# Performance work log

Measured on AMD Instinct MI355X. Metric: run time of the kernel, lower is better.

The kernel has to match this reference:

```python
import jax, jax.numpy as jnp
import numpy as np

B, C, L = 32, 64, 4096
HIDDEN = 64
SR = 50.0
KS = (7, 15, 31, 63)
PHYS = 12
EPS_BN = 1e-5
EPS_GN = 1e-5


def _dwconv(x, w):
    # x: (B,C,L), w: (C,1,k) depthwise kernel, SAME padding for odd k
    k = w.shape[-1]
    p = (k - 1) // 2
    return jax.lax.conv_general_dilated(
        x, w, window_strides=(1,), padding=[(p, p)],
        dimension_numbers=('NCH', 'OIH', 'NCH'),
        feature_group_count=x.shape[1])


def _physics(x):
    b, c, l = x.shape
    svm = jnp.sqrt((x * x).sum(axis=1))                      # (B,L) channel norm
    svm_max = svm.max(axis=-1)
    svm_mean = svm.mean(axis=-1)
    svm_std = jnp.std(svm, axis=-1, ddof=1) + 1e-6           # torch.std is unbiased
    jerk = jnp.diff(x, axis=-1) * SR                         # (B,C,L-1)
    jerk_max = jnp.abs(jerk).max(axis=-1).mean(axis=-1)      # (B,)
    jerk_rate = jnp.diff(jerk, axis=-1) * SR
    jerk_rate_max = jnp.abs(jerk_rate).max(axis=-1).mean(axis=-1)
    sign_changes = (x[:, :, :-1] * x[:, :, 1:] < 0).astype(x.dtype)
    zcr = sign_changes.sum(axis=-1).mean(axis=-1) / l
    thr = (svm_mean + 2.0 * svm_std)[:, None]
    impact_duration = (svm > thr).astype(x.dtype).sum(axis=-1) / l
    hthr = (svm_mean + 3.0 * svm_std)[:, None]
    impact_ratio = (svm > hthr).astype(x.dtype).sum(axis=-1) / l
    free_fall = (svm < (svm_mean - svm_std)[:, None]).astype(x.dtype).sum(axis=-1) / l
    second_half = svm[:, l // 2:]
    post_stillness = jnp.tanh(1.0 / (jnp.std(second_half, axis=-1, ddof=1) + 1e-6))
    third = max(1, l // 3)
    pre_mean = svm[:, :third].mean(axis=-1)
    impact_peak = svm[:, third:2 * third].max(axis=-1)
    post_mean = svm[:, 2 * third:].mean(axis=-1)
    fall_phase = jax.nn.relu(impact_peak - pre_mean) + jax.nn.relu(impact_peak - post_mean)
    fall_phase = fall_phase / (jnp.abs(impact_peak) + 1e-6)
    spectrum = jnp.fft.rfft(x.astype(jnp.float32), axis=-1, norm='ortho')
    power = (jnp.abs(spectrum) ** 2).sum(axis=1)             # (B, L//2+1)
    freqs = jnp.linspace(0.0, 1.0, power.shape[-1], dtype=power.dtype)
    total_power = power.sum(axis=-1) + 1e-6
    spectral_centroid = (power * freqs).sum(axis=-1) / total_power
    high_freq_ratio = jnp.where(freqs > 0.4, power, 0.0).sum(axis=-1) / total_power
    feats = jnp.stack([svm_max, svm_mean, jerk_max, jerk_rate_max, zcr,
                       impact_duration, impact_ratio, post_stillness, free_fall,
                       spectral_centroid, high_freq_ratio, fall_phase], axis=-1)
    return jnp.nan_to_num(feats, nan=0.0, posinf=0.0, neginf=0.0).astype(x.dtype)


def _forward(x, dw_w7, dw_w15, dw_w31, dw_w63, bn_g, bn_b, bn_m, bn_v,
             comp_w1, comp_b1, comp_w2, comp_b2,
             pn_g, pn_b, pn_m, pn_v,
             pe_w1, pe_b1, pe_w2, pe_b2, pg_w, pg_b,
             temperature, gn_g, gn_b, proj_w, proj_b, res_scale):
    # 4 depthwise conv + BN(eval) branches
    branches = []
    for i, w in enumerate((dw_w7, dw_w15, dw_w31, dw_w63)):
        y = _dwconv(x, w)
        y = (y - bn_m[i][None, :, None]) / jnp.sqrt(bn_v[i][None, :, None] + EPS_BN) \
            * bn_g[i][None, :, None] + bn_b[i][None, :, None]
        branches.append(y)
    stacked = jnp.stack(branches, axis=1)                    # (B,4,C,L)
    # complexity net: global avg pool -> MLP
    xm = x.mean(axis=-1)                                     # (B,C)
    h = jax.nn.relu(xm @ comp_w1 + comp_b1)
    complexity_logits = h @ comp_w2 + comp_b2                # (B,4)
    # physics gate
    pf = _physics(x)                                         # (B,12)
    pf = (pf - pn_m) / jnp.sqrt(pn_v + EPS_BN) * pn_g + pn_b
    pe = jax.nn.relu(jax.nn.relu(pf @ pe_w1 + pe_b1) @ pe_w2 + pe_b2)
    physics_weights = jax.nn.sigmoid(pe @ pg_w + pg_b)       # (B,4)
    temp = jnp.maximum(temperature, 0.1)
    weights = jax.nn.softmax(complexity_logits * physics_weights / temp, axis=-1)
    mixed = jnp.einsum('bkcl,bk->bcl', stacked, weights)
    # proj: GroupNorm(1,C) -> GELU(exact) -> 1x1 conv
    mu = mixed.mean(axis=(1, 2), keepdims=True)
    var = mixed.var(axis=(1, 2), keepdims=True)
    gn = (mixed - mu) / jnp.sqrt(var + EPS_GN) * gn_g[None, :, None] + gn_b[None, :, None]
    act = jax.nn.gelu(gn, approximate=False)
    out = jnp.einsum('oc,bcl->bol', proj_w, act) + proj_b[None, :, None]
    return x + res_scale * out


def setup_inputs() -> dict:
    ks = jax.random.split(jax.random.key(0), 16)
    f32 = jnp.float32
    inp = {}
    inp['x'] = jax.random.normal(ks[0], (B, C, L), dtype=f32)
    for i, k in enumerate(KS):
        inp[f'dw_w{k}'] = jax.random.normal(ks[1 + i], (C, 1, k), dtype=f32) / np.sqrt(k)
    inp['bn_g'] = jnp.ones((4, C), f32)
    inp['bn_b'] = jnp.zeros((4, C), f32)
    inp['bn_m'] = 0.1 * jax.random.normal(ks[5], (4, C), dtype=f32)
    inp['bn_v'] = jax.random.uniform(ks[6], (4, C), dtype=f32, minval=0.5, maxval=1.5)
    inp['comp_w1'] = jax.random.normal(ks[7], (C, HIDDEN), dtype=f32) / np.sqrt(C)
    inp['comp_b1'] = jnp.zeros((HIDDEN,), f32)
    inp['comp_w2'] = jax.random.normal(ks[8], (HIDDEN, 4), dtype=f32) / np.sqrt(HIDDEN)
    inp['comp_b2'] = jnp.zeros((4,), f32)
    inp['pn_g'] = jnp.ones((PHYS,), f32)
    inp['pn_b'] = jnp.zeros((PHYS,), f32)
    inp['pn_m'] = 0.1 * jax.random.normal(ks[9], (PHYS,), dtype=f32)
    inp['pn_v'] = jax.random.uniform(ks[10], (PHYS,), dtype=f32, minval=0.5, maxval=1.5)
    inp['pe_w1'] = jax.random.normal(ks[11], (PHYS, 32), dtype=f32) / np.sqrt(PHYS)
    inp['pe_b1'] = jnp.zeros((32,), f32)
    inp['pe_w2'] = jax.random.normal(ks[12], (32, 32), dtype=f32) / np.sqrt(32)
    inp['pe_b2'] = jnp.zeros((32,), f32)
    inp['pg_w'] = jax.random.normal(ks[13], (32, 4), dtype=f32) / np.sqrt(32)
    inp['pg_b'] = jnp.zeros((4,), f32)
    inp['temperature'] = jnp.asarray(1.0, f32)
    inp['gn_g'] = jnp.ones((C,), f32)
    inp['gn_b'] = jnp.zeros((C,), f32)
    inp['proj_w'] = jax.random.normal(ks[14], (C, C), dtype=f32) / np.sqrt(C)
    inp['proj_b'] = jnp.zeros((C,), f32)
    inp['res_scale'] = jnp.asarray(0.5, f32)  # init is 0.0; 0.5 gives a non-trivial output
    return inp


def reference(x, dw_w7, dw_w15, dw_w31, dw_w63, bn_g, bn_b, bn_m, bn_v,
              comp_w1, comp_b1, comp_w2, comp_b2,
              pn_g, pn_b, pn_m, pn_v,
              pe_w1, pe_b1, pe_w2, pe_b2, pg_w, pg_b,
              temperature, gn_g, gn_b, proj_w, proj_b, res_scale):
    return _forward(x, dw_w7, dw_w15, dw_w31, dw_w63, bn_g, bn_b, bn_m, bn_v,
                    comp_w1, comp_b1, comp_w2, comp_b2, pn_g, pn_b, pn_m, pn_v,
                    pe_w1, pe_b1, pe_w2, pe_b2, pg_w, pg_b,
                    temperature, gn_g, gn_b, proj_w, proj_b, res_scale)
```

## Files before the change

### kernel.cpp

```cpp
#include <hip/hip_runtime.h>
#include <math.h>

#define LN 4096
#define CN 64
#define BQ 32
#define NTH 256

#define OFF_CHAN_SUM    0
#define OFF_CHAN_JERK   2048
#define OFF_CHAN_JRATE  4096
#define OFF_CHAN_ZCR    6144
#define OFF_SVMST_PART  8192
#define OFF_SPEC_PART   12288
#define OFF_EFF_B       15360
#define OFF_GNP         17408
#define OFF_EFF_W       21504
#define OFF_SVMBUF      152576

#define FP(i) ((i) + ((i) >> 4))

__device__ __forceinline__ void bfly4(float2& a, float2& b, float2& c, float2& d,
                                      float w1r, float w1i, float w2r, float w2i,
                                      float w3r, float w3i) {
  float t1r = b.x*w1r - b.y*w1i, t1i = b.x*w1i + b.y*w1r;
  float t2r = c.x*w2r - c.y*w2i, t2i = c.x*w2i + c.y*w2r;
  float t3r = d.x*w3r - d.y*w3i, t3i = d.x*w3i + d.y*w3r;
  float ar = a.x + t2r, ai = a.y + t2i;
  float br = a.x - t2r, bi = a.y - t2i;
  float cr = t1r + t3r, ci = t1i + t3i;
  float dr = t1r - t3r, di = t1i - t3i;
  a = make_float2(ar + cr, ai + ci);
  b = make_float2(br + di, bi - dr);
  c = make_float2(ar - cr, ai - ci);
  d = make_float2(br - di, bi + dr);
}

__global__ __launch_bounds__(NTH) void kS(const float* __restrict__ x, float* __restrict__ ws) {
  __shared__ __align__(16) char smraw[34880];
  int role = blockIdx.x;
  int t = threadIdx.x;

  if (role < 2048) {
    int bc = role;
    const float* row = x + (size_t)bc * LN;
    int l0 = t * 16;
    float rd[18];
    const float4* r4 = (const float4*)(row + l0);
#pragma unroll
    for (int q = 0; q < 4; q++) {
      float4 v = r4[q];
      rd[4*q] = v.x; rd[4*q+1] = v.y; rd[4*q+2] = v.z; rd[4*q+3] = v.w;
    }
    if (t < 255) { rd[16] = row[l0 + 16]; rd[17] = row[l0 + 17]; }
    else { rd[16] = 0.f; rd[17] = 0.f; }
    float lsum = 0.f, jm = 0.f, jrm = 0.f; int zc = 0;
#pragma unroll
    for (int i = 0; i < 16; i++) {
      float a = rd[i], b2 = rd[i+1];
      lsum += a;
      int l = l0 + i;
      if (l < LN - 1) {
        jm = fmaxf(jm, fabsf(b2 - a));
        zc += (a * b2 < 0.f);
        if (l < LN - 2) jrm = fmaxf(jrm, fabsf(rd[i+2] - 2.f*b2 + a));
      }
    }
    for (int off = 32; off > 0; off >>= 1) {
      lsum += __shfl_down(lsum, off);
      jm = fmaxf(jm, __shfl_down(jm, off));
      jrm = fmaxf(jrm, __shfl_down(jrm, off));
      zc += __shfl_down(zc, off);
    }
    float* s1 = (float*)smraw; float* s2_ = s1 + 4; float* s3 = s1 + 8; int* s4 = (int*)(s1 + 12);
    int w = t >> 6;
    if ((t & 63) == 0) { s1[w] = lsum; s2_[w] = jm; s3[w] = jrm; s4[w] = zc; }
    __syncthreads();
    if (t == 0) {
      float S = 0, J = 0, JR = 0; int Z = 0;
      for (int i = 0; i < 4; i++) { S += s1[i]; J = fmaxf(J, s2_[i]); JR = fmaxf(JR, s3[i]); Z += s4[i]; }
      ws[OFF_CHAN_SUM + bc]   = S;
      ws[OFF_CHAN_JERK + bc]  = J * 50.f;
      ws[OFF_CHAN_JRATE + bc] = JR * 2500.f;
      ws[OFF_CHAN_ZCR + bc]   = (float)Z;
    }
  } else if (role < 2560) {
    int blk = role - 2048;
    int b = blk >> 4, lt = blk & 15;
    int l = lt * 256 + t;
    const float* xb = x + (size_t)b * CN * LN + l;
    float acc = 0.f;
#pragma unroll
    for (int c = 0; c < CN; c++) { float v = xb[(size_t)c * LN]; acc = fmaf(v, v, acc); }
    float svm = sqrtf(acc);
    ws[OFF_SVMBUF + (size_t)b * LN + l] = svm;
    const int third = LN / 3;
    float vS = svm, vS2 = svm * svm;
    float vS2H  = (l >= LN/2) ? svm : 0.f;
    float vS2H2 = (l >= LN/2) ? svm * svm : 0.f;
    float vPRE  = (l < third) ? svm : 0.f;
    float vPOST = (l >= 2*third) ? svm : 0.f;
    float vMX = svm;
    float vMID = (l >= third && l < 2*third) ? svm : 0.f;
    for (int off = 32; off > 0; off >>= 1) {
      vS += __shfl_down(vS, off); vS2 += __shfl_down(vS2, off);
      vS2H += __shfl_down(vS2H, off); vS2H2 += __shfl_down(vS2H2, off);
      vPRE += __shfl_down(vPRE, off); vPOST += __shfl_down(vPOST, off);
      vMX = fmaxf(vMX, __shfl_down(vMX, off));
      vMID = fmaxf(vMID, __shfl_down(vMID, off));
    }
    float (*red)[4] = (float(*)[4])smraw;
    int w = t >> 6;
    if ((t & 63) == 0) {
      red[0][w] = vS; red[1][w] = vS2; red[2][w] = vMX; red[3][w] = vS2H;
      red[4][w] = vS2H2; red[5][w] = vPRE; red[6][w] = vMID; red[7][w] = vPOST;
    }
    __syncthreads();
    if (t == 0) {
      float* sp = ws + OFF_SVMST_PART + (size_t)blk * 8;
      sp[0] = red[0][0]+red[0][1]+red[0][2]+red[0][3];
      sp[1] = red[1][0]+red[1][1]+red[1][2]+red[1][3];
      sp[2] = fmaxf(fmaxf(red[2][0],red[2][1]),fmaxf(red[2][2],red[2][3]));
      sp[3] = red[3][0]+red[3][1]+red[3][2]+red[3][3];
      sp[4] = red[4][0]+red[4][1]+red[4][2]+red[4][3];
      sp[5] = red[5][0]+red[5][1]+red[5][2]+red[5][3];
      sp[6] = fmaxf(fmaxf(red[6][0],red[6][1]),fmaxf(red[6][2],red[6][3]));
      sp[7] = red[7][0]+red[7][1]+red[7][2]+red[7][3];
    }
  } else {
    int blk = role - 2560;
    int b = blk >> 5, cp = blk & 31;
    const float* r0 = x + ((size_t)b * CN + 2 * cp) * LN;
    const float* r1 = r0 + LN;
    float2* z = (float2*)smraw;
    float (*red)[4] = (float(*)[4])(smraw + 34816);
#pragma unroll
    for (int k = 0; k < 4; k++) {
      int n4 = (k * 256 + t) * 4;
      float4 a = *(const float4*)(r0 + n4);
      float4 c = *(const float4*)(r1 + n4);
      float ar[4] = {a.x, a.y, a.z, a.w}, cr[4] = {c.x, c.y, c.z, c.w};
#pragma unroll
      for (int q = 0; q < 4; q++) {
        unsigned n = (unsigned)(n4 + q);
        unsigned br = __brev(n) >> 20;
        unsigned dr = ((br & 0x555u) << 1) | ((br & 0xAAAu) >> 1);
        z[FP(dr)] = make_float2(ar[q], cr[q]);
      }
    }
    __syncthreads();
    const float c8r[4] = { 1.f, 0.92387953251f, 0.70710678119f, 0.38268343236f };
    const float c8i[4] = { 0.f, -0.38268343236f, -0.70710678119f, -0.92387953251f };
#pragma unroll
    for (int p = 0; p < 3; p++) {
      const int H = (p == 0) ? 1 : (p == 1) ? 16 : 256;
      int r = t & (H - 1);
      int B = ((t / H) * 16 * H) + r;
      float2 E[16];
#pragma unroll
      for (int q = 0; q < 16; q++) E[q] = z[FP(B + q * H)];
      float su, cu;
      sincospif((float)r / (8.0f * (float)H), &su, &cu);
      float ur = cu, ui = -su;
      float u2r = ur*ur - ui*ui, u2i = 2.f*ur*ui;
      float w1r = u2r*u2r - u2i*u2i, w1i = 2.f*u2r*u2i;
      float w2r = w1r*w1r - w1i*w1i, w2i = 2.f*w1r*w1i;
      float w3r = w2r*w1r - w2i*w1i, w3i = w2r*w1i + w2i*w1r;
#pragma unroll
      for (int m = 0; m < 4; m++)
        bfly4(E[4*m], E[4*m+1], E[4*m+2], E[4*m+3], w1r, w1i, w2r, w2i, w3r, w3i);
#pragma unroll
      for (int m = 0; m < 4; m++) {
        float W1r = ur*c8r[m] - ui*c8i[m];
        float W1i = ur*c8i[m] + ui*c8r[m];
        float W2r = W1r*W1r - W1i*W1i, W2i = 2.f*W1r*W1i;
        float W3r = W2r*W1r - W2i*W1i, W3i = W2r*W1i + W2i*W1r;
        bfly4(E[m], E[m+4], E[m+8], E[m+12], W1r, W1i, W2r, W2i, W3r, W3i);
      }
#pragma unroll
      for (int q = 0; q < 16; q++) z[FP(B + q * H)] = E[q];
      __syncthreads();
    }
    float tot = 0.f, cen = 0.f, hi = 0.f;
    for (int k = t; k <= LN / 2; k += NTH) {
      float p;
      if (k == 0 || k == LN / 2) {
        float2 v = z[FP(k)];
        p = v.x * v.x + v.y * v.y;
      } else {
        float2 zk = z[FP(k)], zn = z[FP(LN - k)];
        float a1 = zk.x + zn.x, a2 = zk.y - zn.y, a3 = zk.y + zn.y, a4 = zk.x - zn.x;
        p = 0.25f * (a1*a1 + a2*a2 + a3*a3 + a4*a4);
      }
      p *= (1.0f / LN);
      tot += p;
      cen += p * ((float)k * (1.0f / (LN / 2)));
      if (k >= 820) hi += p;
    }
    for (int off = 32; off > 0; off >>= 1) {
      tot += __shfl_down(tot, off);
      cen += __shfl_down(cen, off);
      hi  += __shfl_down(hi, off);
    }
    int w = t >> 6;
    if ((t & 63) == 0) { red[0][w] = tot; red[1][w] = cen; red[2][w] = hi; }
    __syncthreads();
    if (t == 0) {
      float* sp = ws + OFF_SPEC_PART + (size_t)blk * 3;
      sp[0] = red[0][0]+red[0][1]+red[0][2]+red[0][3];
      sp[1] = red[1][0]+red[1][1]+red[1][2]+red[1][3];
      sp[2] = red[2][0]+red[2][1]+red[2][2]+red[2][3];
    }
  }
}

__global__ __launch_bounds__(NTH) void k4_gate(
    const float* __restrict__ dw7, const float* __restrict__ dw15,
    const float* __restrict__ dw31, const float* __restrict__ dw63,
    const float* __restrict__ bn_g, const float* __restrict__ bn_b,
    const float* __restrict__ bn_m, const float* __restrict__ bn_v,
    const float* __restrict__ comp_w1, const float* __restrict__ comp_b1,
    const float* __restrict__ comp_w2, const float* __restrict__ comp_b2,
    const float* __restrict__ pn_g, const float* __restrict__ pn_b,
    const float* __restrict__ pn_m, const float* __restrict__ pn_v,
    const float* __restrict__ pe_w1, const float* __restrict__ pe_b1,
    const float* __restrict__ pe_w2, const float* __restrict__ pe_b2,
    const float* __restrict__ pg_w, const float* __restrict__ pg_b,
    const float* __restrict__ temperature,
    float* __restrict__ ws)
{
  int b = blockIdx.x, t = threadIdx.x;
  __shared__ float sp8[16][8];
  __shared__ float sp3[32][3];
  __shared__ float stv[10];
  __shared__ float bc2[2];
  __shared__ float xm[64], h[64], pf[12], pe1v[32], pe2v[32], lgts[4], wts[4];
  __shared__ int ri[3][4], cnts[3];
  if (t < 16) {
    const float* p = ws + OFF_SVMST_PART + (size_t)(b * 16 + t) * 8;
#pragma unroll
    for (int i = 0; i < 8; i++) sp8[t][i] = p[i];
  }
  if (t >= 32 && t < 64) {
    int i = t - 32;
    const float* p = ws + OFF_SPEC_PART + (size_t)(b * 32 + i) * 3;
    sp3[i][0] = p[0]; sp3[i][1] = p[1]; sp3[i][2] = p[2];
  }
  __syncthreads();
  if (t == 0) {
    float S=0,S2=0,MX=-1e30f,S2H=0,S2H2=0,PRE=0,MID=-1e30f,POST=0;
    for (int i = 0; i < 16; i++) {
      S += sp8[i][0]; S2 += sp8[i][1]; MX = fmaxf(MX, sp8[i][2]);
      S2H += sp8[i][3]; S2H2 += sp8[i][4]; PRE += sp8[i][5];
      MID = fmaxf(MID, sp8[i][6]); POST += sp8[i][7];
    }
    float tot=0,cen=0,hi=0;
    for (int i = 0; i < 32; i++) { tot += sp3[i][0]; cen += sp3[i][1]; hi += sp3[i][2]; }
    stv[0]=S; stv[1]=S2; stv[2]=MX; stv[3]=S2H; stv[4]=S2H2;
    stv[5]=PRE; stv[6]=MID; stv[7]=POST; stv[8]=cen/(tot+1e-6f); stv[9]=hi/(tot+1e-6f);
    float mean = S * (1.f / LN);
    float var = (S2 - S * S * (1.f / LN)) * (1.f / (LN - 1));
    var = fmaxf(var, 0.f);
    bc2[0] = mean;
    bc2[1] = sqrtf(var) + 1e-6f;
  }
  __syncthreads();
  float mean = bc2[0], stde = bc2[1];
  float thr2 = mean + 2.f * stde, thr3 = mean + 3.f * stde, thrf = mean - stde;
  const float* svm = ws + OFF_SVMBUF + (size_t)b * LN;
  int c2 = 0, c3 = 0, cf = 0;
  for (int l = t; l < LN; l += NTH) {
    float v = svm[l];
    c2 += (v > thr2); c3 += (v > thr3); cf += (v < thrf);
  }
  for (int off = 32; off > 0; off >>= 1) {
    c2 += __shfl_down(c2, off); c3 += __shfl_down(c3, off); cf += __shfl_down(cf, off);
  }
  int w = t >> 6;
  if ((t & 63) == 0) { ri[0][w] = c2; ri[1][w] = c3; ri[2][w] = cf; }
  float j = 0.f, jr = 0.f, zz = 0.f;
  if (t < 64) {
    xm[t] = ws[OFF_CHAN_SUM + b * 64 + t] * (1.0f / LN);
    j  = ws[OFF_CHAN_JERK + b * 64 + t];
    jr = ws[OFF_CHAN_JRATE + b * 64 + t];
    zz = ws[OFF_CHAN_ZCR + b * 64 + t];
    for (int off = 32; off > 0; off >>= 1) {
      j += __shfl_down(j, off); jr += __shfl_down(jr, off); zz += __shfl_down(zz, off);
    }
  }
  __syncthreads();
  if (t == 0) {
    cnts[0] = ri[0][0]+ri[0][1]+ri[0][2]+ri[0][3];
    cnts[1] = ri[1][0]+ri[1][1]+ri[1][2]+ri[1][3];
    cnts[2] = ri[2][0]+ri[2][1]+ri[2][2]+ri[2][3];
    const int third = LN / 3;
    float S2H = stv[3], S2H2 = stv[4];
    float n2 = (float)(LN / 2);
    float var2 = (S2H2 - S2H * S2H / n2) / (n2 - 1.f);
    var2 = fmaxf(var2, 0.f);
    float post_still = tanhf(1.f / (sqrtf(var2) + 1e-6f));
    float pre_mean = stv[5] / (float)third;
    float post_mean = stv[7] / (float)(LN - 2 * third);
    float pk = stv[6];
    float fp = fmaxf(pk - pre_mean, 0.f) + fmaxf(pk - post_mean, 0.f);
    fp = fp / (fabsf(pk) + 1e-6f);
    pf[0] = stv[2];
    pf[1] = mean;
    pf[2] = j * (1.f / 64);
    pf[3] = jr * (1.f / 64);
    pf[4] = (zz * (1.f / 64)) * (1.f / LN);
    pf[5] = (float)cnts[0] / LN;
    pf[6] = (float)cnts[1] / LN;
    pf[7] = post_still;
    pf[8] = (float)cnts[2] / LN;
    pf[9] = stv[8];
    pf[10] = stv[9];
    pf[11] = fp;
  }
  __syncthreads();
  if (t < 12) pf[t] = (pf[t] - pn_m[t]) * rsqrtf(pn_v[t] + 1e-5f) * pn_g[t] + pn_b[t];
  __syncthreads();
  if (t < 64) {
    float hv = comp_b1[t];
    for (int i = 0; i < 64; i++) hv = fmaf(xm[i], comp_w1[i * 64 + t], hv);
    h[t] = fmaxf(hv, 0.f);
  }
  if (t < 32) {
    float v = pe_b1[t];
    for (int i = 0; i < 12; i++) v = fmaf(pf[i], pe_w1[i * 32 + t], v);
    pe1v[t] = fmaxf(v, 0.f);
  }
  __syncthreads();
  if (t < 32) {
    float v = pe_b2[t];
    for (int i = 0; i < 32; i++) v = fmaf(pe1v[i], pe_w2[i * 32 + t], v);
    pe2v[t] = fmaxf(v, 0.f);
  }
  __syncthreads();
  if (t < 4) {
    float v = comp_b2[t];
    for (int i = 0; i < 64; i++) v = fmaf(h[i], comp_w2[i * 4 + t], v);
    float g = pg_b[t];
    for (int i = 0; i < 32; i++) g = fmaf(pe2v[i], pg_w[i * 4 + t], g);
    g = 1.f / (1.f + expf(-g));
    float temp = fmaxf(temperature[0], 0.1f);
    lgts[t] = v * g / temp;
  }
  __syncthreads();
  if (t < 4) {
    float m = fmaxf(fmaxf(lgts[0], lgts[1]), fmaxf(lgts[2], lgts[3]));
    float den = expf(lgts[0]-m) + expf(lgts[1]-m) + expf(lgts[2]-m) + expf(lgts[3]-m);
    wts[t] = expf(lgts[t] - m) / den;
  }
  __syncthreads();
  if (t < 64) {
    int c = t;
    float w0 = wts[0], w1 = wts[1], w2 = wts[2], w3 = wts[3];
    float sc0 = bn_g[0*64+c] * rsqrtf(bn_v[0*64+c] + 1e-5f);
    float sc1 = bn_g[1*64+c] * rsqrtf(bn_v[1*64+c] + 1e-5f);
    float sc2 = bn_g[2*64+c] * rsqrtf(bn_v[2*64+c] + 1e-5f);
    float sc3 = bn_g[3*64+c] * rsqrtf(bn_v[3*64+c] + 1e-5f);
    float o0 = bn_b[0*64+c] - bn_m[0*64+c] * sc0;
    float o1 = bn_b[1*64+c] - bn_m[1*64+c] * sc1;
    float o2 = bn_b[2*64+c] - bn_m[2*64+c] * sc2;
    float o3 = bn_b[3*64+c] - bn_m[3*64+c] * sc3;
    ws[OFF_EFF_B + b * 64 + c] = w0*o0 + w1*o1 + w2*o2 + w3*o3;
    float a0 = w0*sc0, a1 = w1*sc1, a2 = w2*sc2, a3 = w3*sc3;
    float* eff = ws + OFF_EFF_W + (size_t)(b * 64 + c) * 64;
    for (int tau = 0; tau < 64; tau++) {
      float v = 0.f;
      if (tau < 63) {
        v = a3 * dw63[c * 63 + tau];
        int i7 = tau - 28;  if (i7 >= 0 && i7 < 7)   v = fmaf(a0, dw7[c * 7 + i7], v);
        int i15 = tau - 24; if (i15 >= 0 && i15 < 15) v = fmaf(a1, dw15[c * 15 + i15], v);
        int i31 = tau - 16; if (i31 >= 0 && i31 < 31) v = fmaf(a2, dw31[c * 31 + i31], v);
      }
      eff[tau] = v;
    }
  }
}

__device__ __forceinline__ float4 ldmask(const float* __restrict__ row, int idx) {
  int idxc = idx < 0 ? 0 : (idx > LN - 4 ? LN - 4 : idx);
  float4 v = *(const float4*)(row + idxc);
  float m = (idx == idxc) ? 1.f : 0.f;
  v.x *= m; v.y *= m; v.z *= m; v.w *= m;
  return v;
}

#define F16(wv,a0,a1,a2,a3,a4,a5,a6,a7,a8,a9,aA,aB,aC,aD,aE,aF) \
  acc[0]=fmaf(wv,a0,acc[0]);  acc[1]=fmaf(wv,a1,acc[1]);  acc[2]=fmaf(wv,a2,acc[2]);  acc[3]=fmaf(wv,a3,acc[3]);  \
  acc[4]=fmaf(wv,a4,acc[4]);  acc[5]=fmaf(wv,a5,acc[5]);  acc[6]=fmaf(wv,a6,acc[6]);  acc[7]=fmaf(wv,a7,acc[7]);  \
  acc[8]=fmaf(wv,a8,acc[8]);  acc[9]=fmaf(wv,a9,acc[9]);  acc[10]=fmaf(wv,aA,acc[10]); acc[11]=fmaf(wv,aB,acc[11]); \
  acc[12]=fmaf(wv,aC,acc[12]); acc[13]=fmaf(wv,aD,acc[13]); acc[14]=fmaf(wv,aE,acc[14]); acc[15]=fmaf(wv,aF,acc[15]);

__global__ __launch_bounds__(NTH) void k5_conv(const float* __restrict__ x,
                                               float* __restrict__ ws,
                                               float* __restrict__ mixed_out) {
  int bc = blockIdx.x;
  int t = threadIdx.x;
  __shared__ float wt[64];
  __shared__ float biasS;
  __shared__ double rda[2][4];
  if (t < 64) wt[t] = ws[OFF_EFF_W + (size_t)bc * 64 + t];
  if (t == 0) biasS = ws[OFF_EFF_B + bc];
  const float* row = x + (size_t)bc * LN;
  int l0 = t * 16;
  int g0 = l0 - 32;
  float4 R0 = ldmask(row, g0);
  float4 R1 = ldmask(row, g0 + 4);
  float4 R2 = ldmask(row, g0 + 8);
  float4 R3 = ldmask(row, g0 + 12);
  float4 R4 = ldmask(row, g0 + 16);
  __syncthreads();
  float bias = biasS;
  float acc[16];
#pragma unroll
  for (int jj = 0; jj < 16; jj++) acc[jj] = bias;
#pragma unroll
  for (int g = 0; g < 16; g++) {
    float w0 = wt[4*g], w1 = wt[4*g+1], w2 = wt[4*g+2], w3 = wt[4*g+3];
    F16(w0, R0.y,R0.z,R0.w,R1.x,R1.y,R1.z,R1.w,R2.x,R2.y,R2.z,R2.w,R3.x,R3.y,R3.z,R3.w,R4.x)
    F16(w1, R0.z,R0.w,R1.x,R1.y,R1.z,R1.w,R2.x,R2.y,R2.z,R2.w,R3.x,R3.y,R3.z,R3.w,R4.x,R4.y)
    F16(w2, R0.w,R1.x,R1.y,R1.z,R1.w,R2.x,R2.y,R2.z,R2.w,R3.x,R3.y,R3.z,R3.w,R4.x,R4.y,R4.z)
    F16(w3, R1.x,R1.y,R1.z,R1.w,R2.x,R2.y,R2.z,R2.w,R3.x,R3.y,R3.z,R3.w,R4.x,R4.y,R4.z,R4.w)
    if (g < 15) {
      R0 = R1; R1 = R2; R2 = R3; R3 = R4;
      R4 = ldmask(row, g0 + 4 * (g + 5));
    }
  }
  double ls = 0, ls2 = 0;
#pragma unroll
  for (int jj = 0; jj < 16; jj++) { float v = acc[jj]; ls += v; ls2 += (double)v * (double)v; }
  for (int off = 32; off > 0; off >>= 1) {
    ls += __shfl_down(ls, off);
    ls2 += __shfl_down(ls2, off);
  }
  int w = t >> 6;
  if ((t & 63) == 0) { rda[0][w] = ls; rda[1][w] = ls2; }
  __syncthreads();
  if (t == 0) {
    double* gp = (double*)(ws + OFF_GNP);
    gp[2 * bc + 0] = rda[0][0]+rda[0][1]+rda[0][2]+rda[0][3];
    gp[2 * bc + 1] = rda[1][0]+rda[1][1]+rda[1][2]+rda[1][3];
  }
  float* dst = mixed_out + (size_t)bc * LN + l0;
#pragma unroll
  for (int q = 0; q < 4; q++) {
    float4 v; v.x = acc[4*q]; v.y = acc[4*q+1]; v.z = acc[4*q+2]; v.w = acc[4*q+3];
    *(float4*)(dst + 4 * q) = v;
  }
}

__global__ __launch_bounds__(NTH) void k6_final(const float* __restrict__ x,
    const float* __restrict__ proj_w, const float* __restrict__ proj_b,
    const float* __restrict__ gn_g, const float* __restrict__ gn_b,
    const float* __restrict__ res_scale,
    const float* __restrict__ ws, float* out) {
  int blk = blockIdx.x;
  int b = blk >> 5;
  int l0 = (blk & 31) * 128;
  __shared__ float actS[64 * 128];
  __shared__ float Wt[64 * 64];
  __shared__ double rg[2][4];
  __shared__ float bcst[2];
  int t = threadIdx.x;
  {
    const double* gp = (const double*)(ws + OFF_GNP) + (size_t)b * CN * 2;
    double s1 = 0, s2 = 0;
    for (int i = t; i < CN; i += NTH) { s1 += gp[2*i]; s2 += gp[2*i+1]; }
    for (int off = 32; off > 0; off >>= 1) { s1 += __shfl_down(s1, off); s2 += __shfl_down(s2, off); }
    int w = t >> 6;
    if ((t & 63) == 0) { rg[0][w] = s1; rg[1][w] = s2; }
    __syncthreads();
    if (t == 0) {
      double S1 = rg[0][0]+rg[0][1]+rg[0][2]+rg[0][3];
      double S2 = rg[1][0]+rg[1][1]+rg[1][2]+rg[1][3];
      const double NN = 64.0 * 4096.0;
      double mud = S1 / NN;
      bcst[0] = (float)mud;
      bcst[1] = rsqrtf((float)(S2 / NN - mud * mud) + 1e-5f);
    }
  }
  for (int i = t; i < 4096; i += NTH) {
    int o = i & 63, c = i >> 6;
    Wt[c * 64 + o] = proj_w[o * 64 + c];
  }
  __syncthreads();
  float mu = bcst[0], rstd = bcst[1];
  const float* mx = out + (size_t)b * CN * LN;
  for (int i = t; i < 8192; i += NTH) {
    int c = i >> 7, l = i & 127;
    float v = mx[(size_t)c * LN + l0 + l];
    float g = (v - mu) * rstd * gn_g[c] + gn_b[c];
    float a = 0.5f * g * (1.f + erff(g * 0.70710678118654752f));
    actS[c * 128 + l] = a;
  }
  __syncthreads();
  int lg = t & 31;
  int og = (t >> 5) * 8;
  float4 acc4[8];
#pragma unroll
  for (int q = 0; q < 8; q++) { acc4[q].x = 0.f; acc4[q].y = 0.f; acc4[q].z = 0.f; acc4[q].w = 0.f; }
  for (int c = 0; c < 64; c++) {
    float4 a = *(const float4*)&actS[c * 128 + lg * 4];
    float4 wlo = *(const float4*)&Wt[c * 64 + og];
    float4 whi = *(const float4*)&Wt[c * 64 + og + 4];
    float wv[8] = { wlo.x, wlo.y, wlo.z, wlo.w, whi.x, whi.y, whi.z, whi.w };
#pragma unroll
    for (int q = 0; q < 8; q++) {
      acc4[q].x = fmaf(wv[q], a.x, acc4[q].x);
      acc4[q].y = fmaf(wv[q], a.y, acc4[q].y);
      acc4[q].z = fmaf(wv[q], a.z, acc4[q].z);
      acc4[q].w = fmaf(wv[q], a.w, acc4[q].w);
    }
  }
  float rsv = res_scale[0];
  const float* xb = x + (size_t)b * CN * LN;
  float* ob = out + (size_t)b * CN * LN;
#pragma unroll
  for (int q = 0; q < 8; q++) {
    int o = og + q;
    float pb = proj_b[o];
    size_t base = (size_t)o * LN + l0 + lg * 4;
    float4 xv = *(const float4*)&xb[base];
    float4 r;
    r.x = xv.x + rsv * (acc4[q].x + pb);
    r.y = xv.y + rsv * (acc4[q].y + pb);
    r.z = xv.z + rsv * (acc4[q].z + pb);
    r.w = xv.w + rsv * (acc4[q].w + pb);
    *(float4*)&ob[base] = r;
  }
}

extern "C" void kernel_launch(void* const* d_in, const int* in_sizes, int n_in,
                              void* d_out, int out_size, void* d_ws, size_t ws_size,
                              hipStream_t stream) {
  const float* x        = (const float*)d_in[0];
  const float* dw7      = (const float*)d_in[1];
  const float* dw15     = (const float*)d_in[2];
  const float* dw31     = (const float*)d_in[3];
  const float* dw63     = (const float*)d_in[4];
  const float* bn_g     = (const float*)d_in[5];
  const float* bn_b     = (const float*)d_in[6];
  const float* bn_m     = (const float*)d_in[7];
  const float* bn_v     = (const float*)d_in[8];
  const float* comp_w1  = (const float*)d_in[9];
  const float* comp_b1  = (const float*)d_in[10];
  const float* comp_w2  = (const float*)d_in[11];
  const float* comp_b2  = (const float*)d_in[12];
  const float* pn_g     = (const float*)d_in[13];
  const float* pn_b     = (const float*)d_in[14];
  const float* pn_m     = (const float*)d_in[15];
  const float* pn_v     = (const float*)d_in[16];
  const float* pe_w1    = (const float*)d_in[17];
  const float* pe_b1    = (const float*)d_in[18];
  const float* pe_w2    = (const float*)d_in[19];
  const float* pe_b2    = (const float*)d_in[20];
  const float* pg_w     = (const float*)d_in[21];
  const float* pg_b     = (const float*)d_in[22];
  const float* temperature = (const float*)d_in[23];
  const float* gn_g     = (const float*)d_in[24];
  const float* gn_b     = (const float*)d_in[25];
  const float* proj_w   = (const float*)d_in[26];
  const float* proj_b   = (const float*)d_in[27];
  const float* res_scale= (const float*)d_in[28];
  float* ws = (float*)d_ws;
  float* out = (float*)d_out;

  hipLaunchKernelGGL(kS, dim3(2048 + 512 + 1024), dim3(NTH), 0, stream, x, ws);
  hipLaunchKernelGGL(k4_gate, dim3(BQ), dim3(NTH), 0, stream,
                     dw7, dw15, dw31, dw63, bn_g, bn_b, bn_m, bn_v,
                     comp_w1, comp_b1, comp_w2, comp_b2,
                     pn_g, pn_b, pn_m, pn_v, pe_w1, pe_b1, pe_w2, pe_b2,
                     pg_w, pg_b, temperature, ws);
  hipLaunchKernelGGL(k5_conv, dim3(BQ * CN), dim3(NTH), 0, stream, x, ws, out);
  hipLaunchKernelGGL(k6_final, dim3(BQ * 32), dim3(NTH), 0, stream,
                     x, proj_w, proj_b, gn_g, gn_b, res_scale, ws, out);
}
```

Measured before the change: 240.7 us.

## Fuse four kernel launches into one cooperative persistent kernel with grid syncs

Merges the stats, gate, depthwise-conv and final projection kernels into a single cooperative persistent kernel. Blocks loop over work units and grid.sync() separates the stages, which removes launch overhead and the gaps between kernels. In exchange it caps resident blocks, raises shared memory per block to the largest phase's footprint (49 KB), limits occupancy to a few blocks per CU and adds grid-wide barrier cost. The previous multi-kernel path remains as a fallback.

After: 490.5 us. 2.04x slower.

```diff
diff --git a/kernel.cpp b/kernel.cpp
--- a/kernel.cpp
+++ b/kernel.cpp
@@ -1,5 +1,8 @@
 #include <hip/hip_runtime.h>
+#include <hip/hip_cooperative_groups.h>
 #include <math.h>
+
+namespace cg = cooperative_groups;
 
 #define LN 4096
 #define CN 64
@@ -18,6 +21,7 @@
 #define OFF_SVMBUF      152576
 
 #define FP(i) ((i) + ((i) >> 4))
+#define SMBYTES 49280
 
 __device__ __forceinline__ void bfly4(float2& a, float2& b, float2& c, float2& d,
                                       float w1r, float w1i, float w2r, float w2i,
@@ -35,185 +39,183 @@
   d = make_float2(br - di, bi + dr);
 }
 
-__global__ __launch_bounds__(NTH) void kS(const float* __restrict__ x, float* __restrict__ ws) {
-  __shared__ __align__(16) char smraw[34880];
-  int role = blockIdx.x;
-  int t = threadIdx.x;
-
-  if (role < 2048) {
-    int bc = role;
-    const float* row = x + (size_t)bc * LN;
-    int l0 = t * 16;
-    float rd[18];
-    const float4* r4 = (const float4*)(row + l0);
+__device__ __forceinline__ void phase_k1(const float* __restrict__ x, float* __restrict__ ws,
+                                         int bc, char* sm, int t) {
+  const float* row = x + (size_t)bc * LN;
+  int l0 = t * 16;
+  float rd[18];
+  const float4* r4 = (const float4*)(row + l0);
+#pragma unroll
+  for (int q = 0; q < 4; q++) {
+    float4 v = r4[q];
+    rd[4*q] = v.x; rd[4*q+1] = v.y; rd[4*q+2] = v.z; rd[4*q+3] = v.w;
+  }
+  if (t < 255) { rd[16] = row[l0 + 16]; rd[17] = row[l0 + 17]; }
+  else { rd[16] = 0.f; rd[17] = 0.f; }
+  float lsum = 0.f, jm = 0.f, jrm = 0.f; int zc = 0;
+#pragma unroll
+  for (int i = 0; i < 16; i++) {
+    float a = rd[i], b2 = rd[i+1];
+    lsum += a;
+    int l = l0 + i;
+    if (l < LN - 1) {
+      jm = fmaxf(jm, fabsf(b2 - a));
+      zc += (a * b2 < 0.f);
+      if (l < LN - 2) jrm = fmaxf(jrm, fabsf(rd[i+2] - 2.f*b2 + a));
+    }
+  }
+  for (int off = 32; off > 0; off >>= 1) {
+    lsum += __shfl_down(lsum, off);
+    jm = fmaxf(jm, __shfl_down(jm, off));
+    jrm = fmaxf(jrm, __shfl_down(jrm, off));
+    zc += __shfl_down(zc, off);
+  }
+  float* s1 = (float*)sm; float* s2_ = s1 + 4; float* s3 = s1 + 8; int* s4 = (int*)(s1 + 12);
+  int w = t >> 6;
+  if ((t & 63) == 0) { s1[w] = lsum; s2_[w] = jm; s3[w] = jrm; s4[w] = zc; }
+  __syncthreads();
+  if (t == 0) {
+    float S = 0, J = 0, JR = 0; int Z = 0;
+    for (int i = 0; i < 4; i++) { S += s1[i]; J = fmaxf(J, s2_[i]); JR = fmaxf(JR, s3[i]); Z += s4[i]; }
+    ws[OFF_CHAN_SUM + bc]   = S;
+    ws[OFF_CHAN_JERK + bc]  = J * 50.f;
+    ws[OFF_CHAN_JRATE + bc] = JR * 2500.f;
+    ws[OFF_CHAN_ZCR + bc]   = (float)Z;
+  }
+}
+
+__device__ __forceinline__ void phase_kA(const float* __restrict__ x, float* __restrict__ ws,
+                                         int blk, char* sm, int t) {
+  int b = blk >> 4, lt = blk & 15;
+  int l = lt * 256 + t;
+  const float* xb = x + (size_t)b * CN * LN + l;
+  float acc = 0.f;
+#pragma unroll
+  for (int c = 0; c < CN; c++) { float v = xb[(size_t)c * LN]; acc = fmaf(v, v, acc); }
+  float svm = sqrtf(acc);
+  ws[OFF_SVMBUF + (size_t)b * LN + l] = svm;
+  const int third = LN / 3;
+  float vS = svm, vS2 = svm * svm;
+  float vS2H  = (l >= LN/2) ? svm : 0.f;
+  float vS2H2 = (l >= LN/2) ? svm * svm : 0.f;
+  float vPRE  = (l < third) ? svm : 0.f;
+  float vPOST = (l >= 2*third) ? svm : 0.f;
+  float vMX = svm;
+  float vMID = (l >= third && l < 2*third) ? svm : 0.f;
+  for (int off = 32; off > 0; off >>= 1) {
+    vS += __shfl_down(vS, off); vS2 += __shfl_down(vS2, off);
+    vS2H += __shfl_down(vS2H, off); vS2H2 += __shfl_down(vS2H2, off);
+    vPRE += __shfl_down(vPRE, off); vPOST += __shfl_down(vPOST, off);
+    vMX = fmaxf(vMX, __shfl_down(vMX, off));
+    vMID = fmaxf(vMID, __shfl_down(vMID, off));
+  }
+  float (*red)[4] = (float(*)[4])sm;
+  int w = t >> 6;
+  if ((t & 63) == 0) {
+    red[0][w] = vS; red[1][w] = vS2; red[2][w] = vMX; red[3][w] = vS2H;
+    red[4][w] = vS2H2; red[5][w] = vPRE; red[6][w] = vMID; red[7][w] = vPOST;
+  }
+  __syncthreads();
+  if (t == 0) {
+    float* sp = ws + OFF_SVMST_PART + (size_t)blk * 8;
+    sp[0] = red[0][0]+red[0][1]+red[0][2]+red[0][3];
+    sp[1] = red[1][0]+red[1][1]+red[1][2]+red[1][3];
+    sp[2] = fmaxf(fmaxf(red[2][0],red[2][1]),fmaxf(red[2][2],red[2][3]));
+    sp[3] = red[3][0]+red[3][1]+red[3][2]+red[3][3];
+    sp[4] = red[4][0]+red[4][1]+red[4][2]+red[4][3];
+    sp[5] = red[5][0]+red[5][1]+red[5][2]+red[5][3];
+    sp[6] = fmaxf(fmaxf(red[6][0],red[6][1]),fmaxf(red[6][2],red[6][3]));
+    sp[7] = red[7][0]+red[7][1]+red[7][2]+red[7][3];
+  }
+}
+
+__device__ __forceinline__ void phase_fft(const float* __restrict__ x, float* __restrict__ ws,
+                                          int blk, char* sm, int t) {
+  int b = blk >> 5, cp = blk & 31;
+  const float* r0 = x + ((size_t)b * CN + 2 * cp) * LN;
+  const float* r1 = r0 + LN;
+  float2* z = (float2*)sm;
+  float (*red)[4] = (float(*)[4])(sm + 34816);
+#pragma unroll
+  for (int k = 0; k < 4; k++) {
+    int n4 = (k * 256 + t) * 4;
+    float4 a = *(const float4*)(r0 + n4);
+    float4 c = *(const float4*)(r1 + n4);
+    float ar[4] = {a.x, a.y, a.z, a.w}, cr[4] = {c.x, c.y, c.z, c.w};
 #pragma unroll
     for (int q = 0; q < 4; q++) {
-      float4 v = r4[q];
-      rd[4*q] = v.x; rd[4*q+1] = v.y; rd[4*q+2] = v.z; rd[4*q+3] = v.w;
-    }
-    if (t < 255) { rd[16] = row[l0 + 16]; rd[17] = row[l0 + 17]; }
-    else { rd[16] = 0.f; rd[17] = 0.f; }
-    float lsum = 0.f, jm = 0.f, jrm = 0.f; int zc = 0;
-#pragma unroll
-    for (int i = 0; i < 16; i++) {
-      float a = rd[i], b2 = rd[i+1];
-      lsum += a;
-      int l = l0 + i;
-      if (l < LN - 1) {
-        jm = fmaxf(jm, fabsf(b2 - a));
-        zc += (a * b2 < 0.f);
-        if (l < LN - 2) jrm = fmaxf(jrm, fabsf(rd[i+2] - 2.f*b2 + a));
-      }
-    }
-    for (int off = 32; off > 0; off >>= 1) {
-      lsum += __shfl_down(lsum, off);
-      jm = fmaxf(jm, __shfl_down(jm, off));
-      jrm = fmaxf(jrm, __shfl_down(jrm, off));
-      zc += __shfl_down(zc, off);
-    }
-    float* s1 = (float*)smraw; float* s2_ = s1 + 4; float* s3 = s1 + 8; int* s4 = (int*)(s1 + 12);
-    int w = t >> 6;
-    if ((t & 63) == 0) { s1[w] = lsum; s2_[w] = jm; s3[w] = jrm; s4[w] = zc; }
+      unsigned n = (unsigned)(n4 + q);
+      unsigned br = __brev(n) >> 20;
+      unsigned dr = ((br & 0x555u) << 1) | ((br & 0xAAAu) >> 1);
+      z[FP(dr)] = make_float2(ar[q], cr[q]);
+    }
+  }
+  __syncthreads();
+  const float c8r[4] = { 1.f, 0.92387953251f, 0.70710678119f, 0.38268343236f };
+  const float c8i[4] = { 0.f, -0.38268343236f, -0.70710678119f, -0.92387953251f };
+#pragma unroll
+  for (int p = 0; p < 3; p++) {
+    const int H = (p == 0) ? 1 : (p == 1) ? 16 : 256;
+    int r = t & (H - 1);
+    int B = ((t / H) * 16 * H) + r;
+    float2 E[16];
+#pragma unroll
+    for (int q = 0; q < 16; q++) E[q] = z[FP(B + q * H)];
+    float su, cu;
+    sincospif((float)r / (8.0f * (float)H), &su, &cu);
+    float ur = cu, ui = -su;
+    float u2r = ur*ur - ui*ui, u2i = 2.f*ur*ui;
+    float w1r = u2r*u2r - u2i*u2i, w1i = 2.f*u2r*u2i;
+    float w2r = w1r*w1r - w1i*w1i, w2i = 2.f*w1r*w1i;
+    float w3r = w2r*w1r - w2i*w1i, w3i = w2r*w1i + w2i*w1r;
+#pragma unroll
+    for (int m = 0; m < 4; m++)
+      bfly4(E[4*m], E[4*m+1], E[4*m+2], E[4*m+3], w1r, w1i, w2r, w2i, w3r, w3i);
+#pragma unroll
+    for (int m = 0; m < 4; m++) {
+      float W1r = ur*c8r[m] - ui*c8i[m];
+      float W1i = ur*c8i[m] + ui*c8r[m];
+      float W2r = W1r*W1r - W1i*W1i, W2i = 2.f*W1r*W1i;
+      float W3r = W2r*W1r - W2i*W1i, W3i = W2r*W1i + W2i*W1r;
+      bfly4(E[m], E[m+4], E[m+8], E[m+12], W1r, W1i, W2r, W2i, W3r, W3i);
+    }
+#pragma unroll
+    for (int q = 0; q < 16; q++) z[FP(B + q * H)] = E[q];
     __syncthreads();
-    if (t == 0) {
-      float S = 0, J = 0, JR = 0; int Z = 0;
-      for (int i = 0; i < 4; i++) { S += s1[i]; J = fmaxf(J, s2_[i]); JR = fmaxf(JR, s3[i]); Z += s4[i]; }
-      ws[OFF_CHAN_SUM + bc]   = S;
-      ws[OFF_CHAN_JERK + bc]  = J * 50.f;
-      ws[OFF_CHAN_JRATE + bc] = JR * 2500.f;
-      ws[OFF_CHAN_ZCR + bc]   = (float)Z;
-    }
-  } else if (role < 2560) {
-    int blk = role - 2048;
-    int b = blk >> 4, lt = blk & 15;
-    int l = lt * 256 + t;
-    const float* xb = x + (size_t)b * CN * LN + l;
-    float acc = 0.f;
-#pragma unroll
-    for (int c = 0; c < CN; c++) { float v = xb[(size_t)c * LN]; acc = fmaf(v, v, acc); }
-    float svm = sqrtf(acc);
-    ws[OFF_SVMBUF + (size_t)b * LN + l] = svm;
-    const int third = LN / 3;
-    float vS = svm, vS2 = svm * svm;
-    float vS2H  = (l >= LN/2) ? svm : 0.f;
-    float vS2H2 = (l >= LN/2) ? svm * svm : 0.f;
-    float vPRE  = (l < third) ? svm : 0.f;
-    float vPOST = (l >= 2*third) ? svm : 0.f;
-    float vMX = svm;
-    float vMID = (l >= third && l < 2*third) ? svm : 0.f;
-    for (int off = 32; off > 0; off >>= 1) {
-      vS += __shfl_down(vS, off); vS2 += __shfl_down(vS2, off);
-      vS2H += __shfl_down(vS2H, off); vS2H2 += __shfl_down(vS2H2, off);
-      vPRE += __shfl_down(vPRE, off); vPOST += __shfl_down(vPOST, off);
-      vMX = fmaxf(vMX, __shfl_down(vMX, off));
-      vMID = fmaxf(vMID, __shfl_down(vMID, off));
-    }
-    float (*red)[4] = (float(*)[4])smraw;
-    int w = t >> 6;
-    if ((t & 63) == 0) {
-      red[0][w] = vS; red[1][w] = vS2; red[2][w] = vMX; red[3][w] = vS2H;
-      red[4][w] = vS2H2; red[5][w] = vPRE; red[6][w] = vMID; red[7][w] = vPOST;
-    }
-    __syncthreads();
-    if (t == 0) {
-      float* sp = ws + OFF_SVMST_PART + (size_t)blk * 8;
-      sp[0] = red[0][0]+red[0][1]+red[0][2]+red[0][3];
-      sp[1] = red[1][0]+red[1][1]+red[1][2]+red[1][3];
-      sp[2] = fmaxf(fmaxf(red[2][0],red[2][1]),fmaxf(red[2][2],red[2][3]));
-      sp[3] = red[3][0]+red[3][1]+red[3][2]+red[3][3];
-      sp[4] = red[4][0]+red[4][1]+red[4][2]+red[4][3];
-      sp[5] = red[5][0]+red[5][1]+red[5][2]+red[5][3];
-      sp[6] = fmaxf(fmaxf(red[6][0],red[6][1]),fmaxf(red[6][2],red[6][3]));
-      sp[7] = red[7][0]+red[7][1]+red[7][2]+red[7][3];
-    }
-  } else {
-    int blk = role - 2560;
-    int b = blk >> 5, cp = blk & 31;
-    const float* r0 = x + ((size_t)b * CN + 2 * cp) * LN;
-    const float* r1 = r0 + LN;
-    float2* z = (float2*)smraw;
-    float (*red)[4] = (float(*)[4])(smraw + 34816);
-#pragma unroll
-    for (int k = 0; k < 4; k++) {
-      int n4 = (k * 256 + t) * 4;
-      float4 a = *(const float4*)(r0 + n4);
-      float4 c = *(const float4*)(r1 + n4);
-      float ar[4] = {a.x, a.y, a.z, a.w}, cr[4] = {c.x, c.y, c.z, c.w};
-#pragma unroll
-      for (int q = 0; q < 4; q++) {
-        unsigned n = (unsigned)(n4 + q);
-        unsigned br = __brev(n) >> 20;
-        unsigned dr = ((br & 0x555u) << 1) | ((br & 0xAAAu) >> 1);
-        z[FP(dr)] = make_float2(ar[q], cr[q]);
-      }
-    }
-    __syncthreads();
-    const float c8r[4] = { 1.f, 0.92387953251f, 0.70710678119f, 0.38268343236f };
-    const float c8i[4] = { 0.f, -0.38268343236f, -0.70710678119f, -0.92387953251f };
-#pragma unroll
-    for (int p = 0; p < 3; p++) {
-      const int H = (p == 0) ? 1 : (p == 1) ? 16 : 256;
-      int r = t & (H - 1);
-      int B = ((t / H) * 16 * H) + r;
-      float2 E[16];
-#pragma unroll
-      for (int q = 0; q < 16; q++) E[q] = z[FP(B + q * H)];
-      float su, cu;
-      sincospif((float)r / (8.0f * (float)H), &su, &cu);
-      float ur = cu, ui = -su;
-      float u2r = ur*ur - ui*ui, u2i = 2.f*ur*ui;
-      float w1r = u2r*u2r - u2i*u2i, w1i = 2.f*u2r*u2i;
-      float w2r = w1r*w1r - w1i*w1i, w2i = 2.f*w1r*w1i;
-      float w3r = w2r*w1r - w2i*w1i, w3i = w2r*w1i + w2i*w1r;
-#pragma unroll
-      for (int m = 0; m < 4; m++)
-        bfly4(E[4*m], E[4*m+1], E[4*m+2], E[4*m+3], w1r, w1i, w2r, w2i, w3r, w3i);
-#pragma unroll
-      for (int m = 0; m < 4; m++) {
-        float W1r = ur*c8r[m] - ui*c8i[m];
-        float W1i = ur*c8i[m] + ui*c8r[m];
-        float W2r = W1r*W1r - W1i*W1i, W2i = 2.f*W1r*W1i;
-        float W3r = W2r*W1r - W2i*W1i, W3i = W2r*W1i + W2i*W1r;
-        bfly4(E[m], E[m+4], E[m+8], E[m+12], W1r, W1i, W2r, W2i, W3r, W3i);
-      }
-#pragma unroll
-      for (int q = 0; q < 16; q++) z[FP(B + q * H)] = E[q];
-      __syncthreads();
-    }
-    float tot = 0.f, cen = 0.f, hi = 0.f;
-    for (int k = t; k <= LN / 2; k += NTH) {
-      float p;
-      if (k == 0 || k == LN / 2) {
-        float2 v = z[FP(k)];
-        p = v.x * v.x + v.y * v.y;
-      } else {
-        float2 zk = z[FP(k)], zn = z[FP(LN - k)];
-        float a1 = zk.x + zn.x, a2 = zk.y - zn.y, a3 = zk.y + zn.y, a4 = zk.x - zn.x;
-        p = 0.25f * (a1*a1 + a2*a2 + a3*a3 + a4*a4);
-      }
-      p *= (1.0f / LN);
-      tot += p;
-      cen += p * ((float)k * (1.0f / (LN / 2)));
-      if (k >= 820) hi += p;
-    }
-    for (int off = 32; off > 0; off >>= 1) {
-      tot += __shfl_down(tot, off);
-      cen += __shfl_down(cen, off);
-      hi  += __shfl_down(hi, off);
-    }
-    int w = t >> 6;
-    if ((t & 63) == 0) { red[0][w] = tot; red[1][w] = cen; red[2][w] = hi; }
-    __syncthreads();
-    if (t == 0) {
-      float* sp = ws + OFF_SPEC_PART + (size_t)blk * 3;
-      sp[0] = red[0][0]+red[0][1]+red[0][2]+red[0][3];
-      sp[1] = red[1][0]+red[1][1]+red[1][2]+red[1][3];
-      sp[2] = red[2][0]+red[2][1]+red[2][2]+red[2][3];
-    }
-  }
-}
-
-__global__ __launch_bounds__(NTH) void k4_gate(
+  }
+  float tot = 0.f, cen = 0.f, hi = 0.f;
+  for (int k = t; k <= LN / 2; k += NTH) {
+    float p;
+    if (k == 0 || k == LN / 2) {
+      float2 v = z[FP(k)];
+      p = v.x * v.x + v.y * v.y;
+    } else {
+      float2 zk = z[FP(k)], zn = z[FP(LN - k)];
+      float a1 = zk.x + zn.x, a2 = zk.y - zn.y, a3 = zk.y + zn.y, a4 = zk.x - zn.x;
+      p = 0.25f * (a1*a1 + a2*a2 + a3*a3 + a4*a4);
+    }
+    p *= (1.0f / LN);
+    tot += p;
+    cen += p * ((float)k * (1.0f / (LN / 2)));
+    if (k >= 820) hi += p;
+  }
+  for (int off = 32; off > 0; off >>= 1) {
+    tot += __shfl_down(tot, off);
+    cen += __shfl_down(cen, off);
+    hi  += __shfl_down(hi, off);
+  }
+  int w = t >> 6;
+  if ((t & 63) == 0) { red[0][w] = tot; red[1][w] = cen; red[2][w] = hi; }
+  __syncthreads();
+  if (t == 0) {
+    float* sp = ws + OFF_SPEC_PART + (size_t)blk * 3;
+    sp[0] = red[0][0]+red[0][1]+red[0][2]+red[0][3];
+    sp[1] = red[1][0]+red[1][1]+red[1][2]+red[1][3];
+    sp[2] = red[2][0]+red[2][1]+red[2][2]+red[2][3];
+  }
+}
+
+__device__ __forceinline__ void phase_gate(
     const float* __restrict__ dw7, const float* __restrict__ dw15,
     const float* __restrict__ dw31, const float* __restrict__ dw63,
     const float* __restrict__ bn_g, const float* __restrict__ bn_b,
@@ -226,15 +228,21 @@
     const float* __restrict__ pe_w2, const float* __restrict__ pe_b2,
     const float* __restrict__ pg_w, const float* __restrict__ pg_b,
     const float* __restrict__ temperature,
-    float* __restrict__ ws)
+    float* __restrict__ ws, int b, char* sm, int t)
 {
-  int b = blockIdx.x, t = threadIdx.x;
-  __shared__ float sp8[16][8];
-  __shared__ float sp3[32][3];
-  __shared__ float stv[10];
-  __shared__ float bc2[2];
-  __shared__ float xm[64], h[64], pf[12], pe1v[32], pe2v[32], lgts[4], wts[4];
-  __shared__ int ri[3][4], cnts[3];
+  float (*sp8)[8]  = (float(*)[8])sm;
+  float (*sp3)[3]  = (float(*)[3])(sm + 512);
+  float* stv  = (float*)(sm + 896);
+  float* bc2  = (float*)(sm + 936);
+  float* xm   = (float*)(sm + 944);
+  float* h    = (float*)(sm + 1200);
+  float* pf   = (float*)(sm + 1456);
+  float* pe1v = (float*)(sm + 1504);
+  float* pe2v = (float*)(sm + 1632);
+  float* lgts = (float*)(sm + 1760);
+  float* wts  = (float*)(sm + 1776);
+  int (*ri)[4] = (int(*)[4])(sm + 1792);
+  int* cnts = (int*)(sm + 1840);
   if (t < 16) {
     const float* p = ws + OFF_SVMST_PART + (size_t)(b * 16 + t) * 8;
 #pragma unroll
@@ -393,16 +401,13 @@
   acc[8]=fmaf(wv,a8,acc[8]);  acc[9]=fmaf(wv,a9,acc[9]);  acc[10]=fmaf(wv,aA,acc[10]); acc[11]=fmaf(wv,aB,acc[11]); \
   acc[12]=fmaf(wv,aC,acc[12]); acc[13]=fmaf(wv,aD,acc[13]); acc[14]=fmaf(wv,aE,acc[14]); acc[15]=fmaf(wv,aF,acc[15]);
 
-__global__ __launch_bounds__(NTH) void k5_conv(const float* __restrict__ x,
-                                               float* __restrict__ ws,
-                                               float* __restrict__ mixed_out) {
-  int bc = blockIdx.x;
-  int t = threadIdx.x;
-  __shared__ float wt[64];
-  __shared__ float biasS;
-  __shared__ double rda[2][4];
+__device__ __forceinline__ void phase_conv(const float* __restrict__ x, float* __restrict__ ws,
+                                           float* __restrict__ out, int bc, char* sm, int t) {
+  float* wt = (float*)sm;
+  float* biasS = (float*)(sm + 256);
+  double (*rda)[4] = (double(*)[4])(sm + 384);
   if (t < 64) wt[t] = ws[OFF_EFF_W + (size_t)bc * 64 + t];
-  if (t == 0) biasS = ws[OFF_EFF_B + bc];
+  if (t == 0) biasS[0] = ws[OFF_EFF_B + bc];
   const float* row = x + (size_t)bc * LN;
   int l0 = t * 16;
   int g0 = l0 - 32;
@@ -412,7 +417,7 @@
   float4 R3 = ldmask(row, g0 + 12);
   float4 R4 = ldmask(row, g0 + 16);
   __syncthreads();
-  float bias = biasS;
+  float bias = biasS[0];
   float acc[16];
 #pragma unroll
   for (int jj = 0; jj < 16; jj++) acc[jj] = bias;
@@ -443,7 +448,7 @@
     gp[2 * bc + 0] = rda[0][0]+rda[0][1]+rda[0][2]+rda[0][3];
     gp[2 * bc + 1] = rda[1][0]+rda[1][1]+rda[1][2]+rda[1][3];
   }
-  float* dst = mixed_out + (size_t)bc * LN + l0;
+  float* dst = out + (size_t)bc * LN + l0;
 #pragma unroll
   for (int q = 0; q < 4; q++) {
     float4 v; v.x = acc[4*q]; v.y = acc[4*q+1]; v.z = acc[4*q+2]; v.w = acc[4*q+3];
@@ -451,19 +456,17 @@
   }
 }
 
-__global__ __launch_bounds__(NTH) void k6_final(const float* __restrict__ x,
+__device__ __forceinline__ void phase_final(const float* __restrict__ x,
     const float* __restrict__ proj_w, const float* __restrict__ proj_b,
     const float* __restrict__ gn_g, const float* __restrict__ gn_b,
     const float* __restrict__ res_scale,
-    const float* __restrict__ ws, float* out) {
-  int blk = blockIdx.x;
+    const float* __restrict__ ws, float* __restrict__ out, int blk, char* sm, int t) {
   int b = blk >> 5;
   int l0 = (blk & 31) * 128;
-  __shared__ float actS[64 * 128];
-  __shared__ float Wt[64 * 64];
-  __shared__ double rg[2][4];
-  __shared__ float bcst[2];
-  int t = threadIdx.x;
+  float* actS = (float*)sm;
+  float* Wt = (float*)(sm + 32768);
+  double (*rg)[4] = (double(*)[4])(sm + 49152);
+  float* bcst = (float*)(sm + 49216);
   {
     const double* gp = (const double*)(ws + OFF_GNP) + (size_t)b * CN * 2;
     double s1 = 0, s2 = 0;
@@ -530,6 +533,86 @@
     r.w = xv.w + rsv * (acc4[q].w + pb);
     *(float4*)&ob[base] = r;
   }
+}
+
+__global__ __launch_bounds__(NTH, 3) void mega(
+    const float* __restrict__ x,
+    const float* __restrict__ dw7, const float* __restrict__ dw15,
+    const float* __restrict__ dw31, const float* __restrict__ dw63,
+    const float* __restrict__ bn_g, const float* __restrict__ bn_b,
+    const float* __restrict__ bn_m, const float* __restrict__ bn_v,
+    const float* __restrict__ comp_w1, const float* __restrict__ comp_b1,
+    const float* __restrict__ comp_w2, const float* __restrict__ comp_b2,
+    const float* __restrict__ pn_g, const float* __restrict__ pn_b,
+    const float* __restrict__ pn_m, const float* __restrict__ pn_v,
+    const float* __restrict__ pe_w1, const float* __restrict__ pe_b1,
+    const float* __restrict__ pe_w2, const float* __restrict__ pe_b2,
+    const float* __restrict__ pg_w, const float* __restrict__ pg_b,
+    const float* __restrict__ temperature,
+    const float* __restrict__ gn_g, const float* __restrict__ gn_b,
+    const float* __restrict__ proj_w, const float* __restrict__ proj_b,
+    const float* __restrict__ res_scale,
+    float* __restrict__ ws, float* __restrict__ out)
+{
+  __shared__ __align__(16) char sm[SMBYTES];
+  cg::grid_group grid = cg::this_grid();
+  int t = threadIdx.x;
+  int nb = gridDim.x;
+  for (int u = blockIdx.x; u < 3584; u += nb) {
+    if (u < 2048)      phase_k1(x, ws, u, sm, t);
+    else if (u < 2560) phase_kA(x, ws, u - 2048, sm, t);
+    else               phase_fft(x, ws, u - 2560, sm, t);
+    __syncthreads();
+  }
+  grid.sync();
+  if (blockIdx.x < BQ)
+    phase_gate(dw7, dw15, dw31, dw63, bn_g, bn_b, bn_m, bn_v,
+               comp_w1, comp_b1, comp_w2, comp_b2, pn_g, pn_b, pn_m, pn_v,
+               pe_w1, pe_b1, pe_w2, pe_b2, pg_w, pg_b, temperature, ws, blockIdx.x, sm, t);
+  grid.sync();
+  for (int u = blockIdx.x; u < 2048; u += nb) {
+    phase_conv(x, ws, out, u, sm, t);
+    __syncthreads();
+  }
+  grid.sync();
+  for (int u = blockIdx.x; u < 1024; u += nb) {
+    phase_final(x, proj_w, proj_b, gn_g, gn_b, res_scale, ws, out, u, sm, t);
+    __syncthreads();
+  }
+}
+
+__global__ __launch_bounds__(NTH) void kS(const float* __restrict__ x, float* __restrict__ ws) {
+  __shared__ __align__(16) char smraw[SMBYTES];
+  int role = blockIdx.x;
+  int t = threadIdx.x;
+  if (role < 2048)      phase_k1(x, ws, role, smraw, t);
+  else if (role < 2560) phase_kA(x, ws, role - 2048, smraw, t);
+  else                  phase_fft(x, ws, role - 2560, smraw, t);
+}
+
+__global__ __launch_bounds__(NTH) void k4_gate(
+    const float* dw7, const float* dw15, const float* dw31, const float* dw63,
+    const float* bn_g, const float* bn_b, const float* bn_m, const float* bn_v,
+    const float* comp_w1, const float* comp_b1, const float* comp_w2, const float* comp_b2,
+    const float* pn_g, const float* pn_b, const float* pn_m, const float* pn_v,
+    const float* pe_w1, const float* pe_b1, const float* pe_w2, const float* pe_b2,
+    const float* pg_w, const float* pg_b, const float* temperature, float* ws) {
+  __shared__ __align__(16) char smraw[2048];
+  phase_gate(dw7, dw15, dw31, dw63, bn_g, bn_b, bn_m, bn_v,
+             comp_w1, comp_b1, comp_w2, comp_b2, pn_g, pn_b, pn_m, pn_v,
+             pe_w1, pe_b1, pe_w2, pe_b2, pg_w, pg_b, temperature, ws, blockIdx.x, smraw, threadIdx.x);
+}
+
+__global__ __launch_bounds__(NTH) void k5_conv(const float* x, float* ws, float* out) {
+  __shared__ __align__(16) char smraw[512];
+  phase_conv(x, ws, out, blockIdx.x, smraw, threadIdx.x);
+}
+
+__global__ __launch_bounds__(NTH) void k6_final(const float* x,
+    const float* proj_w, const float* proj_b, const float* gn_g, const float* gn_b,
+    const float* res_scale, const float* ws, float* out) {
+  __shared__ __align__(16) char smraw[SMBYTES];
+  phase_final(x, proj_w, proj_b, gn_g, gn_b, res_scale, ws, out, blockIdx.x, smraw, threadIdx.x);
 }
 
 extern "C" void kernel_launch(void* const* d_in, const int* in_sizes, int n_in,
@@ -567,6 +650,26 @@
   float* ws = (float*)d_ws;
   float* out = (float*)d_out;
 
+  int maxB = 0;
+  hipError_t occ_err = hipOccupancyMaxActiveBlocksPerMultiprocessor(&maxB, mega, NTH, 0);
+  bool coop_ok = (occ_err == hipSuccess && maxB >= 1);
+  if (coop_ok) {
+    int nblk = maxB * 256;
+    if (nblk > 2048) nblk = 2048;
+    void* kargs[] = {
+      (void*)&x, (void*)&dw7, (void*)&dw15, (void*)&dw31, (void*)&dw63,
+      (void*)&bn_g, (void*)&bn_b, (void*)&bn_m, (void*)&bn_v,
+      (void*)&comp_w1, (void*)&comp_b1, (void*)&comp_w2, (void*)&comp_b2,
+      (void*)&pn_g, (void*)&pn_b, (void*)&pn_m, (void*)&pn_v,
+      (void*)&pe_w1, (void*)&pe_b1, (void*)&pe_w2, (void*)&pe_b2,
+      (void*)&pg_w, (void*)&pg_b, (void*)&temperature,
+      (void*)&gn_g, (void*)&gn_b, (void*)&proj_w, (void*)&proj_b, (void*)&res_scale,
+      (void*)&ws, (void*)&out
+    };
+    hipError_t lerr = hipLaunchCooperativeKernel((const void*)mega, dim3(nblk), dim3(NTH),
+                                                 kargs, 0, stream);
+    if (lerr == hipSuccess) return;
+  }
   hipLaunchKernelGGL(kS, dim3(2048 + 512 + 1024), dim3(NTH), 0, stream, x, ws);
   hipLaunchKernelGGL(k4_gate, dim3(BQ), dim3(NTH), 0, stream,
                      dw7, dw15, dw31, dw63, bn_g, bn_b, bn_m, bn_v,
```
